# Performance work log

Measured on AMD Instinct MI355X. Metric: run time of the kernel, lower is better.

Reference implementation:

```python
import jax, jax.numpy as jnp
import numpy as np

N_NODES = 50000
DIM = 128
NEG_SLOPE = 0.2


def _gat_conv(x, W, a_src, a_dst, b, src, dst, n):
    # PyG GATConv, single head, self-loops already appended to (src, dst).
    h = x @ W.T                              # [N, D]
    asrc = h @ a_src                         # [N]
    adst = h @ a_dst                         # [N]
    e = jax.nn.leaky_relu(asrc[src] + adst[dst], NEG_SLOPE)  # [E]
    emax = jax.ops.segment_max(e, dst, num_segments=n)
    emax = jnp.where(jnp.isfinite(emax), emax, 0.0)
    ex = jnp.exp(e - emax[dst])
    denom = jax.ops.segment_sum(ex, dst, num_segments=n)
    coef = ex / (denom[dst] + 1e-16)         # segment softmax over incoming edges
    out = jax.ops.segment_sum(coef[:, None] * h[src], dst, num_segments=n)
    return out + b


def _l2norm(x):
    # F.normalize(x) row-wise, eps=1e-12
    n = jnp.sqrt(jnp.sum(x * x, axis=1, keepdims=True))
    return x / jnp.maximum(n, 1e-12)


def setup_inputs() -> dict:
    key = jax.random.key(0)
    ks = jax.random.split(key, 24)
    d = DIM
    inp = {
        'entity_feat_1': jax.random.normal(ks[0], (N_NODES, d), jnp.float32),
        'image_feat': jax.random.normal(ks[1], (N_NODES, 4096), jnp.float32),
        'text_feat': jax.random.normal(ks[2], (N_NODES, 768), jnp.float32),
        'graph_edges': jax.random.randint(ks[3], (2, 600000), 0, N_NODES, jnp.int64),
        'entity_feat': jax.random.normal(ks[4], (N_NODES, d), jnp.float32) * (6.0 / (N_NODES + d)) ** 0.5 * 100,
        'W_img': jax.random.normal(ks[5], (d, 4096), jnp.float32) * 0.02,
        'b_img': jnp.zeros((d,), jnp.float32),
        'W_txt': jax.random.normal(ks[6], (d, 768), jnp.float32) * 0.03,
        'b_txt': jnp.zeros((d,), jnp.float32),
        'W_fus': jax.random.normal(ks[7], (d, 3 * d), jnp.float32) * 0.05,
        'b_fus': jnp.zeros((d,), jnp.float32),
    }
    for i, tag in enumerate(['e', 'i', 't']):
        base = 8 + 4 * i
        inp['W%s_gat' % tag] = jax.random.normal(ks[base], (d, d), jnp.float32) * 0.08
        inp['a%s_src' % tag] = jax.random.normal(ks[base + 1], (d,), jnp.float32) * 0.1
        inp['a%s_dst' % tag] = jax.random.normal(ks[base + 2], (d,), jnp.float32) * 0.1
        inp['b%s_gat' % tag] = jnp.zeros((d,), jnp.float32)
    return inp


def reference(entity_feat_1, image_feat, text_feat, graph_edges, entity_feat,
              W_img, b_img, W_txt, b_txt, W_fus, b_fus,
              We_gat, ae_src, ae_dst, be_gat,
              Wi_gat, ai_src, ai_dst, bi_gat,
              Wt_gat, at_src, at_dst, bt_gat):
    n = entity_feat.shape[0]
    loops = jnp.arange(n, dtype=graph_edges.dtype)
    src = jnp.concatenate([graph_edges[0], loops])
    dst = jnp.concatenate([graph_edges[1], loops])
    img = image_feat @ W_img.T + b_img
    txt = text_feat @ W_txt.T + b_txt
    # GraphConv = GATConv -> dropout(eval: identity) -> F.normalize
    e_out = _l2norm(_gat_conv(entity_feat, We_gat, ae_src, ae_dst, be_gat, src, dst, n))
    i_out = _l2norm(_gat_conv(img, Wi_gat, ai_src, ai_dst, bi_gat, src, dst, n))
    t_out = _l2norm(_gat_conv(txt, Wt_gat, at_src, at_dst, bt_gat, src, dst, n))
    mm = jnp.concatenate([e_out, i_out, t_out], axis=1) @ W_fus.T + b_fus
    return (e_out, i_out, t_out, mm)
```

## Files before the change

kernel.cpp:

```cpp
#include <hip/hip_runtime.h>
#include <hip/hip_bf16.h>

typedef __attribute__((ext_vector_type(8))) short bf16x8;
typedef __attribute__((ext_vector_type(4))) short bf16x4;
typedef __attribute__((ext_vector_type(4))) float f32x4;

#define LDS_A2 16384
#define LDS_HALF2 32768

__device__ __forceinline__ float fin(float v) {
    return (v == v && v > -1e30f && v < 1e30f) ? v : 0.f;
}
__device__ __forceinline__ float lrelu(float v) {
    return (v >= 0.f) ? v : 0.2f * v;
}
__device__ __forceinline__ unsigned f2bu(float f) {
    unsigned u = __builtin_bit_cast(unsigned, f);
    return (u + 0x7FFFu + ((u >> 16) & 1u)) >> 16;
}
__device__ __forceinline__ short f2b(float f) { return (short)f2bu(f); }
__device__ __forceinline__ float bflo(unsigned u) {
    return __builtin_bit_cast(float, u << 16);
}
__device__ __forceinline__ float bfhi(unsigned u) {
    return __builtin_bit_cast(float, u & 0xffff0000u);
}

template<int FUSE, int AD, int HP, int NT, int AF16, int OUT16>
__device__ __forceinline__
void gemm_body(const float* __restrict__ A0, const float* __restrict__ A1,
               const float* __restrict__ A2, const __hip_bfloat16* __restrict__ A16,
               const __hip_bfloat16* __restrict__ Bw,
               const float* __restrict__ bias,
               const float* __restrict__ av1, const float* __restrict__ av2,
               float* __restrict__ asrc, float* __restrict__ adst, int astride,
               float* __restrict__ Cf, __hip_bfloat16* __restrict__ C16,
               unsigned* __restrict__ Cp,
               int M, int K, int bx)
{
    __shared__ __align__(16) char smem[2][LDS_HALF2];
    const int tid = threadIdx.x;
    const int l  = tid & 63;
    const int lr = l & 15;
    const int lk = l >> 4;
    const int w  = tid >> 6;
    const int brow = bx * 128;
    const int nt = K >> 6;

    f32x4 acc[8];
#pragma unroll
    for (int j = 0; j < 8; j++) acc[j] = (f32x4){0.f, 0.f, 0.f, 0.f};

    f32x4 va[4];
    bf16x8 va16[2], vb16[2];

    auto stage_load = [&](int t) {
        const int k0 = t << 6;
        if (AF16) {
#pragma unroll
            for (int i = 0; i < 2; i++) {
                int elem = (i * 512 + tid) * 8;
                int row = elem >> 6;
                int col = elem & 63;
                int gr = brow + row; if (gr >= M) gr = M - 1;
                va16[i] = *(const bf16x8*)(A16 + (size_t)gr * (size_t)K + k0 + col);
            }
        } else {
#pragma unroll
            for (int i = 0; i < 4; i++) {
                int elem = (i * 512 + tid) * 4;
                int row = elem >> 6;
                int col = elem & 63;
                int gr = brow + row; if (gr >= M) gr = M - 1;
                int gcol = k0 + col;
                const float* p;
                if (FUSE) {
                    int seg = gcol >> 7;
                    const float* s = (seg == 0) ? A0 : (seg == 1) ? A1 : A2;
                    p = s + (size_t)gr * 128 + (gcol & 127);
                } else {
                    p = A0 + (size_t)gr * (size_t)K + gcol;
                }
                va[i] = NT ? __builtin_nontemporal_load((const f32x4*)p)
                           : *(const f32x4*)p;
            }
        }
#pragma unroll
        for (int i = 0; i < 2; i++) {
            int elem = (i * 512 + tid) * 8;
            int row = elem >> 6;
            int col = elem & 63;
            vb16[i] = *(const bf16x8*)(Bw + (size_t)row * (size_t)K + k0 + col);
        }
    };
    auto stage_write = [&](int buf) {
        if (AF16) {
#pragma unroll
            for (int i = 0; i < 2; i++) {
                int elem = (i * 512 + tid) * 8;
                int row = elem >> 6;
                int col = elem & 63;
                int slo = (col * 2) ^ ((row & 7) << 4);
                *(bf16x8*)(&smem[buf][row * 128 + slo]) = va16[i];
            }
        } else {
#pragma unroll
            for (int i = 0; i < 4; i++) {
                int elem = (i * 512 + tid) * 4;
                int row = elem >> 6;
                int col = elem & 63;
                int slo = (col * 2) ^ ((row & 7) << 4);
                bf16x4 a4 = {f2b(va[i].x), f2b(va[i].y), f2b(va[i].z), f2b(va[i].w)};
                *(bf16x4*)(&smem[buf][row * 128 + slo]) = a4;
            }
        }
#pragma unroll
        for (int i = 0; i < 2; i++) {
            int elem = (i * 512 + tid) * 8;
            int row = elem >> 6;
            int col = elem & 63;
            int slo = (col * 2) ^ ((row & 7) << 4);
            *(bf16x8*)(&smem[buf][LDS_A2 + row * 128 + slo]) = vb16[i];
        }
    };

    stage_load(0);
    stage_write(0);
    __syncthreads();
    int cur = 0;
    for (int t = 0; t < nt; t++) {
        if (t + 1 < nt) stage_load(t + 1);
        const char* Ab = &smem[cur][0];
        const char* Bb = &smem[cur][LDS_A2];
#pragma unroll
        for (int ks = 0; ks < 2; ks++) {
            bf16x8 af, bv[8];
            {
                int row = w * 16 + lr;
                int lo  = (ks * 64 + lk * 16) ^ ((row & 7) << 4);
                af = *(const bf16x8*)(Ab + row * 128 + lo);
            }
#pragma unroll
            for (int nf = 0; nf < 8; nf++) {
                int row = nf * 16 + lr;
                int lo  = (ks * 64 + lk * 16) ^ ((row & 7) << 4);
                bv[nf] = *(const bf16x8*)(Bb + row * 128 + lo);
            }
#pragma unroll
            for (int nf = 0; nf < 8; nf++)
                acc[nf] = __builtin_amdgcn_mfma_f32_16x16x32_bf16(
                    af, bv[nf], acc[nf], 0, 0, 0);
        }
        if (t + 1 < nt) stage_write(cur ^ 1);
        __syncthreads();
        cur ^= 1;
    }

#pragma unroll
    for (int j = 0; j < 4; j++) {
        int row = brow + w * 16 + lk * 4 + j;
        float vv[8];
        float s1 = 0.f, s2 = 0.f;
#pragma unroll
        for (int nf = 0; nf < 8; nf++) {
            int col = nf * 16 + lr;
            float v = acc[nf][j];
            if (bias) v += bias[col];
            v = fin(v);
            vv[nf] = v;
            if (AD) { s1 += v * av1[col]; s2 += v * av2[col]; }
            if (!HP && !OUT16 && row < M) Cf[(size_t)row * 128 + col] = v;
            if (OUT16 && row < M)
                C16[(size_t)row * 128 + col] = __builtin_bit_cast(__hip_bfloat16, f2b(v));
        }
        if (HP && row < M) {
#pragma unroll
            for (int nf = 0; nf < 4; nf++) {
                int col = nf * 16 + lr;
                Cp[(size_t)row * 64 + col] = f2bu(vv[nf]) | (f2bu(vv[nf + 4]) << 16);
            }
        }
        if (AD) {
#pragma unroll
            for (int o = 1; o < 16; o <<= 1) {
                s1 += __shfl_xor(s1, o);
                s2 += __shfl_xor(s2, o);
            }
            if (lr == 0 && row < M) {
                asrc[(size_t)row * astride] = fin(s1);
                adst[(size_t)row * astride] = fin(s2);
            }
        }
    }
}

__global__ __launch_bounds__(512, 4)
void gemm_o16(const float* __restrict__ A0, const __hip_bfloat16* __restrict__ Bw,
              const float* __restrict__ bias, __hip_bfloat16* __restrict__ C16,
              int M, int K)
{
    gemm_body<0, 0, 0, 1, 0, 1>(A0, nullptr, nullptr, nullptr, Bw, bias,
                                nullptr, nullptr, nullptr, nullptr, 1,
                                nullptr, C16, nullptr, M, K, blockIdx.x);
}

__global__ __launch_bounds__(512, 4)
void gemm_fus(const float* __restrict__ A0, const float* __restrict__ A1,
              const float* __restrict__ A2, const __hip_bfloat16* __restrict__ Bw,
              const float* __restrict__ bias, float* __restrict__ Cf, int M)
{
    gemm_body<1, 0, 0, 0, 0, 0>(A0, A1, A2, nullptr, Bw, bias,
                                nullptr, nullptr, nullptr, nullptr, 1,
                                Cf, nullptr, nullptr, M, 384, blockIdx.x);
}

__global__ __launch_bounds__(512, 4)
void hgemm3(const float* __restrict__ x0, const __hip_bfloat16* __restrict__ x1,
            const __hip_bfloat16* __restrict__ x2,
            const __hip_bfloat16* __restrict__ w0, const __hip_bfloat16* __restrict__ w1,
            const __hip_bfloat16* __restrict__ w2,
            const float* __restrict__ a10, const float* __restrict__ a11,
            const float* __restrict__ a12,
            const float* __restrict__ a20, const float* __restrict__ a21,
            const float* __restrict__ a22,
            unsigned* __restrict__ cp0, unsigned* __restrict__ cp1,
            unsigned* __restrict__ cp2,
            float* __restrict__ asrc4, float* __restrict__ adst4, int M)
{
    int g = blockIdx.y;
    if (g == 0)
        gemm_body<0, 1, 1, 1, 0, 0>(x0, nullptr, nullptr, nullptr, w0, nullptr,
                                    a10, a20, asrc4 + 0, adst4 + 0, 4,
                                    nullptr, nullptr, cp0, M, 128, blockIdx.x);
    else if (g == 1)
        gemm_body<0, 1, 1, 0, 1, 0>(nullptr, nullptr, nullptr, x1, w1, nullptr,
                                    a11, a21, asrc4 + 1, adst4 + 1, 4,
                                    nullptr, nullptr, cp1, M, 128, blockIdx.x);
    else
        gemm_body<0, 1, 1, 0, 1, 0>(nullptr, nullptr, nullptr, x2, w2, nullptr,
                                    a12, a22, asrc4 + 2, adst4 + 2, 4,
                                    nullptr, nullptr, cp2, M, 128, blockIdx.x);
}

__global__ void k_cvt6(const float* __restrict__ s0, const float* __restrict__ s1,
                       const float* __restrict__ s2, const float* __restrict__ s3,
                       const float* __restrict__ s4, const float* __restrict__ s5,
                       __hip_bfloat16* __restrict__ d0, __hip_bfloat16* __restrict__ d1,
                       __hip_bfloat16* __restrict__ d2, __hip_bfloat16* __restrict__ d3,
                       __hip_bfloat16* __restrict__ d4, __hip_bfloat16* __restrict__ d5,
                       int n0, int n1, int n2, int n3, int n4, int n5)
{
    int g = blockIdx.y;
    const float* s = (g == 0) ? s0 : (g == 1) ? s1 : (g == 2) ? s2
                   : (g == 3) ? s3 : (g == 4) ? s4 : s5;
    __hip_bfloat16* d = (g == 0) ? d0 : (g == 1) ? d1 : (g == 2) ? d2
                      : (g == 3) ? d3 : (g == 4) ? d4 : d5;
    int n = (g == 0) ? n0 : (g == 1) ? n1 : (g == 2) ? n2
          : (g == 3) ? n3 : (g == 4) ? n4 : n5;
    for (int i = blockIdx.x * blockDim.x + threadIdx.x; i * 4 < n;
         i += gridDim.x * blockDim.x) {
        f32x4 v = *(const f32x4*)(s + (size_t)i * 4);
        bf16x4 b = {f2b(v.x), f2b(v.y), f2b(v.z), f2b(v.w)};
        *(bf16x4*)((short*)d + (size_t)i * 4) = b;
    }
}

__global__ void k_init(const int* __restrict__ e, int* __restrict__ flag,
                       int* __restrict__ deg, int* __restrict__ cursor, int n)
{
    if (blockIdx.x == 0 && threadIdx.x < 64) {
        int v = e[2 * threadIdx.x + 1];
        unsigned long long b = __ballot(v != 0);
        if (threadIdx.x == 0) flag[0] = (b == 0ull) ? 1 : 0;
    }
    for (int i = blockIdx.x * blockDim.x + threadIdx.x; i < n;
         i += gridDim.x * blockDim.x) {
        deg[i] = 0;
        cursor[i] = 0;
    }
}

__global__ void k_degree(const int* __restrict__ e, const int* __restrict__ flag,
                         int* __restrict__ deg, int e0, int n)
{
    int i = blockIdx.x * blockDim.x + threadIdx.x;
    if (i >= e0 + n) return;
    int d;
    if (i < e0) d = flag[0] ? e[2 * e0 + 2 * i] : e[e0 + i];
    else        d = i - e0;
    if ((unsigned)d >= (unsigned)n) d = 0;
    atomicAdd(&deg[d], 1);
}

__global__ void k_scan1(const int* __restrict__ deg, int* __restrict__ csum, int n)
{
    __shared__ int sh[512];
    int c = blockIdx.x, t = threadIdx.x, i = c * 512 + t;
    sh[t] = (i < n) ? deg[i] : 0;
    __syncthreads();
    for (int o = 256; o; o >>= 1) {
        if (t < o) sh[t] += sh[t + o];
        __syncthreads();
    }
    if (t == 0) csum[c] = sh[0];
}

__global__ void k_scan2(const int* __restrict__ csum, int* __restrict__ coff,
                        int nc, int* __restrict__ indptr, int n, int total)
{
    __shared__ int sh[128];
    int t = threadIdx.x;
    int v = (t < nc) ? csum[t] : 0;
    sh[t] = v;
    __syncthreads();
    for (int o = 1; o < 128; o <<= 1) {
        int add = (t >= o) ? sh[t - o] : 0;
        __syncthreads();
        sh[t] += add;
        __syncthreads();
    }
    if (t < nc) coff[t] = sh[t] - v;
    if (t == 0) indptr[n] = total;
}

__global__ void k_scan3(const int* __restrict__ deg, const int* __restrict__ coff,
                        int* __restrict__ indptr, int n)
{
    __shared__ int sh[512];
    int c = blockIdx.x, t = threadIdx.x, i = c * 512 + t;
    int v = (i < n) ? deg[i] : 0;
    sh[t] = v;
    __syncthreads();
    for (int o = 1; o < 512; o <<= 1) {
        int add = (t >= o) ? sh[t - o] : 0;
        __syncthreads();
        sh[t] += add;
        __syncthreads();
    }
    if (i < n) indptr[i] = coff[c] + sh[t] - v;
}

__global__ void k_scatter(const int* __restrict__ e, const int* __restrict__ flag,
                          const int* __restrict__ indptr,
                          int* __restrict__ cursor, int* __restrict__ csr,
                          int e0, int n)
{
    int i = blockIdx.x * blockDim.x + threadIdx.x;
    if (i >= e0 + n) return;
    int s, d;
    if (i < e0) {
        if (flag[0]) { s = e[2 * i]; d = e[2 * e0 + 2 * i]; }
        else         { s = e[i];     d = e[e0 + i]; }
    } else {
        s = d = i - e0;
    }
    if ((unsigned)d >= (unsigned)n) d = 0;
    if ((unsigned)s >= (unsigned)n) s = 0;
    int pos = atomicAdd(&cursor[d], 1);
    csr[indptr[d] + pos] = s;
}

__global__ __launch_bounds__(256)
void gat3(const int* __restrict__ indptr, const int* __restrict__ csr,
          const unsigned* __restrict__ hpE, const unsigned* __restrict__ hpI,
          const unsigned* __restrict__ hpT,
          const float* __restrict__ asrc4, const float* __restrict__ adst4,
          const float* __restrict__ bE, const float* __restrict__ bI,
          const float* __restrict__ bT,
          float* __restrict__ oE, float* __restrict__ oI, float* __restrict__ oT,
          int n)
{
    int node = blockIdx.x * 4 + (threadIdx.x >> 6);
    if (node >= n) return;
    int l = threadIdx.x & 63;
    int beg = indptr[node], end = indptr[node + 1];
    int deg_n = end - beg;
    float adE = adst4[(size_t)node * 4 + 0];
    float adI = adst4[(size_t)node * 4 + 1];
    float adT = adst4[(size_t)node * 4 + 2];
    float aE0 = 0.f, aE1 = 0.f, aI0 = 0.f, aI1 = 0.f, aT0 = 0.f, aT1 = 0.f;

    if (deg_n <= 64) {
        int t = beg + l;
        bool valid = t < end;
        int sidx = valid ? csr[t] : 0;
        if ((unsigned)sidx >= (unsigned)n) sidx = 0;
        float eE = -1e30f, eI = -1e30f, eT = -1e30f;
        if (valid) {
            const float* ap = asrc4 + (size_t)sidx * 4;
            eE = lrelu(ap[0] + adE);
            eI = lrelu(ap[1] + adI);
            eT = lrelu(ap[2] + adT);
        }
        float mE = eE, mI = eI, mT = eT;
        for (int o = 32; o; o >>= 1) {
            mE = fmaxf(mE, __shfl_xor(mE, o));
            mI = fmaxf(mI, __shfl_xor(mI, o));
            mT = fmaxf(mT, __shfl_xor(mT, o));
        }
        float xE = valid ? __expf(eE - mE) : 0.f;
        float xI = valid ? __expf(eI - mI) : 0.f;
        float xT = valid ? __expf(eT - mT) : 0.f;
        float sE = xE, sI = xI, sT = xT;
        for (int o = 32; o; o >>= 1) {
            sE += __shfl_xor(sE, o);
            sI += __shfl_xor(sI, o);
            sT += __shfl_xor(sT, o);
        }
        float iE = 1.f / (sE + 1e-16f);
        float iI = 1.f / (sI + 1e-16f);
        float iT = 1.f / (sT + 1e-16f);
        for (int j = 0; j < deg_n; j++) {
            int   sj = __shfl(sidx, j);
            float cE = __shfl(xE, j) * iE;
            float cI = __shfl(xI, j) * iI;
            float cT = __shfl(xT, j) * iT;
            unsigned uE = hpE[(size_t)sj * 64 + l];
            unsigned uI = hpI[(size_t)sj * 64 + l];
            unsigned uT = hpT[(size_t)sj * 64 + l];
            aE0 += cE * bflo(uE); aE1 += cE * bfhi(uE);
            aI0 += cI * bflo(uI); aI1 += cI * bfhi(uI);
            aT0 += cT * bflo(uT); aT1 += cT * bfhi(uT);
        }
    } else {
        const unsigned* hp[3] = {hpE, hpI, hpT};
        float ad3[3] = {adE, adI, adT};
        float* acc0[3] = {&aE0, &aI0, &aT0};
        float* acc1[3] = {&aE1, &aI1, &aT1};
        for (int g = 0; g < 3; g++) {
            float m = -1e30f;
            for (int t = beg + l; t < end; t += 64) {
                int sidx = csr[t];
                if ((unsigned)sidx >= (unsigned)n) sidx = 0;
                m = fmaxf(m, lrelu(asrc4[(size_t)sidx * 4 + g] + ad3[g]));
            }
            for (int o = 32; o; o >>= 1) m = fmaxf(m, __shfl_xor(m, o));
            float s = 0.f;
            for (int t = beg + l; t < end; t += 64) {
                int sidx = csr[t];
                if ((unsigned)sidx >= (unsigned)n) sidx = 0;
                s += __expf(lrelu(asrc4[(size_t)sidx * 4 + g] + ad3[g]) - m);
            }
            for (int o = 32; o; o >>= 1) s += __shfl_xor(s, o);
            float inv = 1.f / (s + 1e-16f);
            for (int t = beg; t < end; t++) {
                int sidx = csr[t];
                if ((unsigned)sidx >= (unsigned)n) sidx = 0;
                float c = __expf(lrelu(asrc4[(size_t)sidx * 4 + g] + ad3[g]) - m) * inv;
                unsigned u = hp[g][(size_t)sidx * 64 + l];
                *acc0[g] += c * bflo(u);
                *acc1[g] += c * bfhi(u);
            }
        }
    }

    {
        float a0 = aE0 + bE[l], a1 = aE1 + bE[64 + l];
        float ss = a0 * a0 + a1 * a1;
        for (int o = 32; o; o >>= 1) ss += __shfl_xor(ss, o);
        float r = 1.f / fmaxf(sqrtf(fin(ss)), 1e-12f);
        oE[(size_t)node * 128 + l]      = fin(a0 * r);
        oE[(size_t)node * 128 + 64 + l] = fin(a1 * r);
    }
    {
        float a0 = aI0 + bI[l], a1 = aI1 + bI[64 + l];
        float ss = a0 * a0 + a1 * a1;
        for (int o = 32; o; o >>= 1) ss += __shfl_xor(ss, o);
        float r = 1.f / fmaxf(sqrtf(fin(ss)), 1e-12f);
        oI[(size_t)node * 128 + l]      = fin(a0 * r);
        oI[(size_t)node * 128 + 64 + l] = fin(a1 * r);
    }
    {
        float a0 = aT0 + bT[l], a1 = aT1 + bT[64 + l];
        float ss = a0 * a0 + a1 * a1;
        for (int o = 32; o; o >>= 1) ss += __shfl_xor(ss, o);
        float r = 1.f / fmaxf(sqrtf(fin(ss)), 1e-12f);
        oT[(size_t)node * 128 + l]      = fin(a0 * r);
        oT[(size_t)node * 128 + 64 + l] = fin(a1 * r);
    }
}

extern "C" void kernel_launch(void* const* d_in, const int* in_sizes, int n_in,
                              void* d_out, int out_size, void* d_ws, size_t ws_size,
                              hipStream_t stream)
{
    int s0 = n_in - 22;
    if (s0 < 0 || s0 > 1)
        s0 = (in_sizes[1] > in_sizes[0]) ? 1 : 0;

    const float* image_feat  = (const float*)d_in[s0 + 0];
    const float* text_feat   = (const float*)d_in[s0 + 1];
    const int*   edges       = (const int*)d_in[s0 + 2];
    const float* entity_feat = (const float*)d_in[s0 + 3];
    const float* W_img = (const float*)d_in[s0 + 4];
    const float* b_img = (const float*)d_in[s0 + 5];
    const float* W_txt = (const float*)d_in[s0 + 6];
    const float* b_txt = (const float*)d_in[s0 + 7];
    const float* W_fus = (const float*)d_in[s0 + 8];
    const float* b_fus = (const float*)d_in[s0 + 9];
    const float* Wg[3]  = {(const float*)d_in[s0 + 10], (const float*)d_in[s0 + 14],
                           (const float*)d_in[s0 + 18]};
    const float* Avv[3] = {(const float*)d_in[s0 + 11], (const float*)d_in[s0 + 15],
                           (const float*)d_in[s0 + 19]};
    const float* Dvv[3] = {(const float*)d_in[s0 + 12], (const float*)d_in[s0 + 16],
                           (const float*)d_in[s0 + 20]};
    const float* Bg[3]  = {(const float*)d_in[s0 + 13], (const float*)d_in[s0 + 17],
                           (const float*)d_in[s0 + 21]};

    const int n  = in_sizes[s0 + 3] / 128;
    int e0 = in_sizes[s0 + 2] / 2;
    if (e0 == 24 * n) e0 = 12 * n;
    const int ne = e0 + n;
    const int Kimg = in_sizes[s0 + 4] / 128;
    const int Ktxt = in_sizes[s0 + 6] / 128;

    char* ws = (char*)d_ws;
    size_t off = 0;
    auto alloc = [&](size_t b) { size_t o = off; off = (off + b + 255) & ~(size_t)255; return o; };
    int* eflag  = (int*)(ws + alloc(256));
    int* deg    = (int*)(ws + alloc((size_t)n * 4));
    int* indptr = (int*)(ws + alloc((size_t)(n + 1) * 4));
    int* cursor = (int*)(ws + alloc((size_t)n * 4));
    int* csum   = (int*)(ws + alloc(512));
    int* coff   = (int*)(ws + alloc(512));
    float* asrc4 = (float*)(ws + alloc((size_t)n * 16));
    float* adst4 = (float*)(ws + alloc((size_t)n * 16));
    int* csr    = (int*)(ws + alloc((size_t)ne * 4));
    __hip_bfloat16* Wimgb = (__hip_bfloat16*)(ws + alloc((size_t)Kimg * 128 * 2));
    __hip_bfloat16* Wtxtb = (__hip_bfloat16*)(ws + alloc((size_t)Ktxt * 128 * 2));
    __hip_bfloat16* Wgb[3];
    for (int g = 0; g < 3; g++) Wgb[g] = (__hip_bfloat16*)(ws + alloc(128 * 128 * 2));
    __hip_bfloat16* Wfusb = (__hip_bfloat16*)(ws + alloc(384 * 128 * 2));
    __hip_bfloat16* imgp16 = (__hip_bfloat16*)(ws + alloc((size_t)n * 128 * 2));
    __hip_bfloat16* txtp16 = (__hip_bfloat16*)(ws + alloc((size_t)n * 128 * 2));
    unsigned* hp[3];
    for (int g = 0; g < 3; g++) hp[g] = (unsigned*)(ws + alloc((size_t)n * 64 * 4));
    (void)ws_size; (void)out_size;

    float* out = (float*)d_out;
    float* oE = out;
    float* oI = out + (size_t)n * 128;
    float* oT = out + 2 * (size_t)n * 128;
    float* oM = out + 3 * (size_t)n * 128;

    k_init<<<208, 256, 0, stream>>>(edges, eflag, deg, cursor, n);
    k_cvt6<<<dim3(128, 6), 256, 0, stream>>>(
        W_img, W_txt, Wg[0], Wg[1], Wg[2], W_fus,
        Wimgb, Wtxtb, Wgb[0], Wgb[1], Wgb[2], Wfusb,
        Kimg * 128, Ktxt * 128, 128 * 128, 128 * 128, 128 * 128, 384 * 128);
    k_degree<<<(ne + 255) / 256, 256, 0, stream>>>(edges, eflag, deg, e0, n);
    const int nch = (n + 511) / 512;
    k_scan1<<<nch, 512, 0, stream>>>(deg, csum, n);
    k_scan2<<<1, 128, 0, stream>>>(csum, coff, nch, indptr, n, ne);
    k_scan3<<<nch, 512, 0, stream>>>(deg, coff, indptr, n);
    k_scatter<<<(ne + 255) / 256, 256, 0, stream>>>(edges, eflag, indptr, cursor, csr, e0, n);

    const int mb = (n + 127) / 128;
    gemm_o16<<<mb, 512, 0, stream>>>(image_feat, Wimgb, b_img, imgp16, n, Kimg);
    gemm_o16<<<mb, 512, 0, stream>>>(text_feat, Wtxtb, b_txt, txtp16, n, Ktxt);

    hgemm3<<<dim3(mb, 3), 512, 0, stream>>>(entity_feat, imgp16, txtp16,
                                            Wgb[0], Wgb[1], Wgb[2],
                                            Avv[0], Avv[1], Avv[2],
                                            Dvv[0], Dvv[1], Dvv[2],
                                            hp[0], hp[1], hp[2],
                                            asrc4, adst4, n);

    gat3<<<(n + 3) / 4, 256, 0, stream>>>(indptr, csr, hp[0], hp[1], hp[2],
                                          asrc4, adst4, Bg[0], Bg[1], Bg[2],
                                          oE, oI, oT, n);

    gemm_fus<<<mb, 512, 0, stream>>>(oE, oI, oT, Wfusb, b_fus, oM, n);
}
```

Baseline: 437.7 us.

## Compose projection and GAT weights to fuse the two GEMM stages into one

Precomputes Wg·W_img and Wg·W_txt (and the composed biases) on device, so the GAT linear transform for the image and text branches runs straight from the raw features in a single GEMM launch. This removes the intermediate bf16 projection buffers and the second GEMM pass over them. The three per-branch h buffers are also interleaved into one 192-word-per-node layout so the GAT gather reads one contiguous region per source node. The trade-offs are an added weight-composition kernel and different rounding, since the intermediate projection is no longer rounded to bf16. The large image and text GEMMs now share one launch grid with the small entity GEMM.

```diff
diff --git a/kernel.cpp b/kernel.cpp
--- a/kernel.cpp
+++ b/kernel.cpp
@@ -26,16 +26,15 @@
     return __builtin_bit_cast(float, u & 0xffff0000u);
 }
 
-template<int FUSE, int AD, int HP, int NT, int AF16, int OUT16>
+template<int FUSE, int AD, int HP, int NT>
 __device__ __forceinline__
 void gemm_body(const float* __restrict__ A0, const float* __restrict__ A1,
-               const float* __restrict__ A2, const __hip_bfloat16* __restrict__ A16,
+               const float* __restrict__ A2,
                const __hip_bfloat16* __restrict__ Bw,
                const float* __restrict__ bias,
                const float* __restrict__ av1, const float* __restrict__ av2,
                float* __restrict__ asrc, float* __restrict__ adst, int astride,
-               float* __restrict__ Cf, __hip_bfloat16* __restrict__ C16,
-               unsigned* __restrict__ Cp,
+               float* __restrict__ Cf, unsigned* __restrict__ Cp, int cpstride,
                int M, int K, int bx)
 {
     __shared__ __align__(16) char smem[2][LDS_HALF2];
@@ -52,38 +51,27 @@
     for (int j = 0; j < 8; j++) acc[j] = (f32x4){0.f, 0.f, 0.f, 0.f};
 
     f32x4 va[4];
-    bf16x8 va16[2], vb16[2];
+    bf16x8 vb16[2];
 
     auto stage_load = [&](int t) {
         const int k0 = t << 6;
-        if (AF16) {
-#pragma unroll
-            for (int i = 0; i < 2; i++) {
-                int elem = (i * 512 + tid) * 8;
-                int row = elem >> 6;
-                int col = elem & 63;
-                int gr = brow + row; if (gr >= M) gr = M - 1;
-                va16[i] = *(const bf16x8*)(A16 + (size_t)gr * (size_t)K + k0 + col);
-            }
-        } else {
-#pragma unroll
-            for (int i = 0; i < 4; i++) {
-                int elem = (i * 512 + tid) * 4;
-                int row = elem >> 6;
-                int col = elem & 63;
-                int gr = brow + row; if (gr >= M) gr = M - 1;
-                int gcol = k0 + col;
-                const float* p;
-                if (FUSE) {
-                    int seg = gcol >> 7;
-                    const float* s = (seg == 0) ? A0 : (seg == 1) ? A1 : A2;
-                    p = s + (size_t)gr * 128 + (gcol & 127);
-                } else {
-                    p = A0 + (size_t)gr * (size_t)K + gcol;
-                }
-                va[i] = NT ? __builtin_nontemporal_load((const f32x4*)p)
-                           : *(const f32x4*)p;
-            }
+#pragma unroll
+        for (int i = 0; i < 4; i++) {
+            int elem = (i * 512 + tid) * 4;
+            int row = elem >> 6;
+            int col = elem & 63;
+            int gr = brow + row; if (gr >= M) gr = M - 1;
+            int gcol = k0 + col;
+            const float* p;
+            if (FUSE) {
+                int seg = gcol >> 7;
+                const float* s = (seg == 0) ? A0 : (seg == 1) ? A1 : A2;
+                p = s + (size_t)gr * 128 + (gcol & 127);
+            } else {
+                p = A0 + (size_t)gr * (size_t)K + gcol;
+            }
+            va[i] = NT ? __builtin_nontemporal_load((const f32x4*)p)
+                       : *(const f32x4*)p;
         }
 #pragma unroll
         for (int i = 0; i < 2; i++) {
@@ -94,25 +82,14 @@
         }
     };
     auto stage_write = [&](int buf) {
-        if (AF16) {
-#pragma unroll
-            for (int i = 0; i < 2; i++) {
-                int elem = (i * 512 + tid) * 8;
-                int row = elem >> 6;
-                int col = elem & 63;
-                int slo = (col * 2) ^ ((row & 7) << 4);
-                *(bf16x8*)(&smem[buf][row * 128 + slo]) = va16[i];
-            }
-        } else {
-#pragma unroll
-            for (int i = 0; i < 4; i++) {
-                int elem = (i * 512 + tid) * 4;
-                int row = elem >> 6;
-                int col = elem & 63;
-                int slo = (col * 2) ^ ((row & 7) << 4);
-                bf16x4 a4 = {f2b(va[i].x), f2b(va[i].y), f2b(va[i].z), f2b(va[i].w)};
-                *(bf16x4*)(&smem[buf][row * 128 + slo]) = a4;
-            }
+#pragma unroll
+        for (int i = 0; i < 4; i++) {
+            int elem = (i * 512 + tid) * 4;
+            int row = elem >> 6;
+            int col = elem & 63;
+            int slo = (col * 2) ^ ((row & 7) << 4);
+            bf16x4 a4 = {f2b(va[i].x), f2b(va[i].y), f2b(va[i].z), f2b(va[i].w)};
+            *(bf16x4*)(&smem[buf][row * 128 + slo]) = a4;
         }
 #pragma unroll
         for (int i = 0; i < 2; i++) {
@@ -169,15 +146,13 @@
             v = fin(v);
             vv[nf] = v;
             if (AD) { s1 += v * av1[col]; s2 += v * av2[col]; }
-            if (!HP && !OUT16 && row < M) Cf[(size_t)row * 128 + col] = v;
-            if (OUT16 && row < M)
-                C16[(size_t)row * 128 + col] = __builtin_bit_cast(__hip_bfloat16, f2b(v));
+            if (!HP && row < M) Cf[(size_t)row * 128 + col] = v;
         }
         if (HP && row < M) {
 #pragma unroll
             for (int nf = 0; nf < 4; nf++) {
                 int col = nf * 16 + lr;
-                Cp[(size_t)row * 64 + col] = f2bu(vv[nf]) | (f2bu(vv[nf + 4]) << 16);
+                Cp[(size_t)row * cpstride + col] = f2bu(vv[nf]) | (f2bu(vv[nf + 4]) << 16);
             }
         }
         if (AD) {
@@ -195,13 +170,30 @@
 }
 
 __global__ __launch_bounds__(512, 4)
-void gemm_o16(const float* __restrict__ A0, const __hip_bfloat16* __restrict__ Bw,
-              const float* __restrict__ bias, __hip_bfloat16* __restrict__ C16,
-              int M, int K)
-{
-    gemm_body<0, 0, 0, 1, 0, 1>(A0, nullptr, nullptr, nullptr, Bw, bias,
-                                nullptr, nullptr, nullptr, nullptr, 1,
-                                nullptr, C16, nullptr, M, K, blockIdx.x);
+void hgemm3b(const float* __restrict__ x0, const float* __restrict__ x1,
+             const float* __restrict__ x2,
+             const __hip_bfloat16* __restrict__ w0,
+             const __hip_bfloat16* __restrict__ w1,
+             const __hip_bfloat16* __restrict__ w2,
+             const float* __restrict__ bc1, const float* __restrict__ bc2,
+             const float* __restrict__ a10, const float* __restrict__ a11,
+             const float* __restrict__ a12,
+             const float* __restrict__ a20, const float* __restrict__ a21,
+             const float* __restrict__ a22,
+             unsigned* __restrict__ hpAll,
+             float* __restrict__ asrc4, float* __restrict__ adst4,
+             int M, int K0, int K1, int K2)
+{
+    int g = blockIdx.y;
+    const float* x  = (g == 0) ? x0 : (g == 1) ? x1 : x2;
+    const __hip_bfloat16* wv = (g == 0) ? w0 : (g == 1) ? w1 : w2;
+    const float* bias = (g == 0) ? nullptr : (g == 1) ? bc1 : bc2;
+    const float* av1 = (g == 0) ? a10 : (g == 1) ? a11 : a12;
+    const float* av2 = (g == 0) ? a20 : (g == 1) ? a21 : a22;
+    int K = (g == 0) ? K0 : (g == 1) ? K1 : K2;
+    gemm_body<0, 1, 1, 1>(x, nullptr, nullptr, wv, bias, av1, av2,
+                          asrc4 + g, adst4 + g, 4,
+                          nullptr, hpAll + g * 64, 192, M, K, blockIdx.x);
 }
 
 __global__ __launch_bounds__(512, 4)
@@ -209,54 +201,66 @@
               const float* __restrict__ A2, const __hip_bfloat16* __restrict__ Bw,
               const float* __restrict__ bias, float* __restrict__ Cf, int M)
 {
-    gemm_body<1, 0, 0, 0, 0, 0>(A0, A1, A2, nullptr, Bw, bias,
-                                nullptr, nullptr, nullptr, nullptr, 1,
-                                Cf, nullptr, nullptr, M, 384, blockIdx.x);
-}
-
-__global__ __launch_bounds__(512, 4)
-void hgemm3(const float* __restrict__ x0, const __hip_bfloat16* __restrict__ x1,
-            const __hip_bfloat16* __restrict__ x2,
-            const __hip_bfloat16* __restrict__ w0, const __hip_bfloat16* __restrict__ w1,
-            const __hip_bfloat16* __restrict__ w2,
-            const float* __restrict__ a10, const float* __restrict__ a11,
-            const float* __restrict__ a12,
-            const float* __restrict__ a20, const float* __restrict__ a21,
-            const float* __restrict__ a22,
-            unsigned* __restrict__ cp0, unsigned* __restrict__ cp1,
-            unsigned* __restrict__ cp2,
-            float* __restrict__ asrc4, float* __restrict__ adst4, int M)
+    gemm_body<1, 0, 0, 0>(A0, A1, A2, Bw, bias, nullptr, nullptr,
+                          nullptr, nullptr, 1, Cf, nullptr, 1, M, 384, blockIdx.x);
+}
+
+__global__ __launch_bounds__(256)
+void k_compose(const float* __restrict__ Wg1, const float* __restrict__ Wb1,
+               const float* __restrict__ bb1, __hip_bfloat16* __restrict__ Wc1,
+               float* __restrict__ bc1, int K1,
+               const float* __restrict__ Wg2, const float* __restrict__ Wb2,
+               const float* __restrict__ bb2, __hip_bfloat16* __restrict__ Wc2,
+               float* __restrict__ bc2, int K2)
+{
+    int y = blockIdx.y;
+    const float* Wg  = y ? Wg2 : Wg1;
+    const float* Wb  = y ? Wb2 : Wb1;
+    const float* bb  = y ? bb2 : bb1;
+    __hip_bfloat16* Wc = y ? Wc2 : Wc1;
+    float* bc = y ? bc2 : bc1;
+    int Kbig = y ? K2 : K1;
+    int tid = threadIdx.x;
+
+    if (blockIdx.x == gridDim.x - 1) {
+        __shared__ float bs[128];
+        if (tid < 128) bs[tid] = bb[tid];
+        __syncthreads();
+        if (tid < 128) {
+            float s = 0.f;
+            for (int m = 0; m < 128; m++) s = fmaf(Wg[tid * 128 + m], bs[m], s);
+            bc[tid] = fin(s);
+        }
+        return;
+    }
+    __shared__ float WgL[128 * 128];
+    for (int i = tid; i < 128 * 128; i += 256) WgL[i] = Wg[i];
+    __syncthreads();
+    int j = blockIdx.x * 64 + (tid & 63);
+    if (j >= Kbig) return;
+    int g = tid >> 6;
+    float acc[32];
+#pragma unroll
+    for (int i = 0; i < 32; i++) acc[i] = 0.f;
+    for (int k = 0; k < 128; k++) {
+        float wvv = Wb[(size_t)k * Kbig + j];
+#pragma unroll
+        for (int i = 0; i < 32; i++)
+            acc[i] = fmaf(WgL[(g * 32 + i) * 128 + k], wvv, acc[i]);
+    }
+#pragma unroll
+    for (int i = 0; i < 32; i++)
+        *((short*)Wc + (size_t)(g * 32 + i) * Kbig + j) = f2b(acc[i]);
+}
+
+__global__ void k_cvt2(const float* __restrict__ s0, const float* __restrict__ s1,
+                       __hip_bfloat16* __restrict__ d0, __hip_bfloat16* __restrict__ d1,
+                       int n0, int n1)
 {
     int g = blockIdx.y;
-    if (g == 0)
-        gemm_body<0, 1, 1, 1, 0, 0>(x0, nullptr, nullptr, nullptr, w0, nullptr,
-                                    a10, a20, asrc4 + 0, adst4 + 0, 4,
-                                    nullptr, nullptr, cp0, M, 128, blockIdx.x);
-    else if (g == 1)
-        gemm_body<0, 1, 1, 0, 1, 0>(nullptr, nullptr, nullptr, x1, w1, nullptr,
-                                    a11, a21, asrc4 + 1, adst4 + 1, 4,
-                                    nullptr, nullptr, cp1, M, 128, blockIdx.x);
-    else
-        gemm_body<0, 1, 1, 0, 1, 0>(nullptr, nullptr, nullptr, x2, w2, nullptr,
-                                    a12, a22, asrc4 + 2, adst4 + 2, 4,
-                                    nullptr, nullptr, cp2, M, 128, blockIdx.x);
-}
-
-__global__ void k_cvt6(const float* __restrict__ s0, const float* __restrict__ s1,
-                       const float* __restrict__ s2, const float* __restrict__ s3,
-                       const float* __restrict__ s4, const float* __restrict__ s5,
-                       __hip_bfloat16* __restrict__ d0, __hip_bfloat16* __restrict__ d1,
-                       __hip_bfloat16* __restrict__ d2, __hip_bfloat16* __restrict__ d3,
-                       __hip_bfloat16* __restrict__ d4, __hip_bfloat16* __restrict__ d5,
-                       int n0, int n1, int n2, int n3, int n4, int n5)
-{
-    int g = blockIdx.y;
-    const float* s = (g == 0) ? s0 : (g == 1) ? s1 : (g == 2) ? s2
-                   : (g == 3) ? s3 : (g == 4) ? s4 : s5;
-    __hip_bfloat16* d = (g == 0) ? d0 : (g == 1) ? d1 : (g == 2) ? d2
-                      : (g == 3) ? d3 : (g == 4) ? d4 : d5;
-    int n = (g == 0) ? n0 : (g == 1) ? n1 : (g == 2) ? n2
-          : (g == 3) ? n3 : (g == 4) ? n4 : n5;
+    const float* s = g ? s1 : s0;
+    __hip_bfloat16* d = g ? d1 : d0;
+    int n = g ? n1 : n0;
     for (int i = blockIdx.x * blockDim.x + threadIdx.x; i * 4 < n;
          i += gridDim.x * blockDim.x) {
         f32x4 v = *(const f32x4*)(s + (size_t)i * 4);
@@ -362,8 +366,7 @@
 
 __global__ __launch_bounds__(256)
 void gat3(const int* __restrict__ indptr, const int* __restrict__ csr,
-          const unsigned* __restrict__ hpE, const unsigned* __restrict__ hpI,
-          const unsigned* __restrict__ hpT,
+          const unsigned* __restrict__ hpAll,
           const float* __restrict__ asrc4, const float* __restrict__ adst4,
           const float* __restrict__ bE, const float* __restrict__ bI,
           const float* __restrict__ bT,
@@ -415,15 +418,15 @@
             float cE = __shfl(xE, j) * iE;
             float cI = __shfl(xI, j) * iI;
             float cT = __shfl(xT, j) * iT;
-            unsigned uE = hpE[(size_t)sj * 64 + l];
-            unsigned uI = hpI[(size_t)sj * 64 + l];
-            unsigned uT = hpT[(size_t)sj * 64 + l];
+            const unsigned* hb = hpAll + (size_t)sj * 192;
+            unsigned uE = hb[l];
+            unsigned uI = hb[64 + l];
+            unsigned uT = hb[128 + l];
             aE0 += cE * bflo(uE); aE1 += cE * bfhi(uE);
             aI0 += cI * bflo(uI); aI1 += cI * bfhi(uI);
             aT0 += cT * bflo(uT); aT1 += cT * bfhi(uT);
         }
     } else {
-        const unsigned* hp[3] = {hpE, hpI, hpT};
         float ad3[3] = {adE, adI, adT};
         float* acc0[3] = {&aE0, &aI0, &aT0};
         float* acc1[3] = {&aE1, &aI1, &aT1};
@@ -447,7 +450,7 @@
                 int sidx = csr[t];
                 if ((unsigned)sidx >= (unsigned)n) sidx = 0;
                 float c = __expf(lrelu(asrc4[(size_t)sidx * 4 + g] + ad3[g]) - m) * inv;
-                unsigned u = hp[g][(size_t)sidx * 64 + l];
+                unsigned u = hpAll[(size_t)sidx * 192 + g * 64 + l];
                 *acc0[g] += c * bflo(u);
                 *acc1[g] += c * bfhi(u);
             }
@@ -526,15 +529,13 @@
     float* asrc4 = (float*)(ws + alloc((size_t)n * 16));
     float* adst4 = (float*)(ws + alloc((size_t)n * 16));
     int* csr    = (int*)(ws + alloc((size_t)ne * 4));
-    __hip_bfloat16* Wimgb = (__hip_bfloat16*)(ws + alloc((size_t)Kimg * 128 * 2));
-    __hip_bfloat16* Wtxtb = (__hip_bfloat16*)(ws + alloc((size_t)Ktxt * 128 * 2));
-    __hip_bfloat16* Wgb[3];
-    for (int g = 0; g < 3; g++) Wgb[g] = (__hip_bfloat16*)(ws + alloc(128 * 128 * 2));
+    __hip_bfloat16* Wgb0  = (__hip_bfloat16*)(ws + alloc(128 * 128 * 2));
     __hip_bfloat16* Wfusb = (__hip_bfloat16*)(ws + alloc(384 * 128 * 2));
-    __hip_bfloat16* imgp16 = (__hip_bfloat16*)(ws + alloc((size_t)n * 128 * 2));
-    __hip_bfloat16* txtp16 = (__hip_bfloat16*)(ws + alloc((size_t)n * 128 * 2));
-    unsigned* hp[3];
-    for (int g = 0; g < 3; g++) hp[g] = (unsigned*)(ws + alloc((size_t)n * 64 * 4));
+    __hip_bfloat16* Wcimg = (__hip_bfloat16*)(ws + alloc((size_t)Kimg * 128 * 2));
+    __hip_bfloat16* Wctxt = (__hip_bfloat16*)(ws + alloc((size_t)Ktxt * 128 * 2));
+    float* bcimg = (float*)(ws + alloc(512));
+    float* bctxt = (float*)(ws + alloc(512));
+    unsigned* hpAll = (unsigned*)(ws + alloc((size_t)n * 192 * 4));
     (void)ws_size; (void)out_size;
 
     float* out = (float*)d_out;
@@ -544,10 +545,11 @@
     float* oM = out + 3 * (size_t)n * 128;
 
     k_init<<<208, 256, 0, stream>>>(edges, eflag, deg, cursor, n);
-    k_cvt6<<<dim3(128, 6), 256, 0, stream>>>(
-        W_img, W_txt, Wg[0], Wg[1], Wg[2], W_fus,
-        Wimgb, Wtxtb, Wgb[0], Wgb[1], Wgb[2], Wfusb,
-        Kimg * 128, Ktxt * 128, 128 * 128, 128 * 128, 128 * 128, 384 * 128);
+    k_cvt2<<<dim3(64, 2), 256, 0, stream>>>(Wg[0], W_fus, Wgb0, Wfusb,
+                                            128 * 128, 384 * 128);
+    k_compose<<<dim3(Kimg / 64 + 1, 2), 256, 0, stream>>>(
+        Wg[1], W_img, b_img, Wcimg, bcimg, Kimg,
+        Wg[2], W_txt, b_txt, Wctxt, bctxt, Ktxt);
     k_degree<<<(ne + 255) / 256, 256, 0, stream>>>(edges, eflag, deg, e0, n);
     const int nch = (n + 511) / 512;
     k_scan1<<<nch, 512, 0, stream>>>(deg, csum, n);
@@ -556,17 +558,14 @@
     k_scatter<<<(ne + 255) / 256, 256, 0, stream>>>(edges, eflag, indptr, cursor, csr, e0, n);
 
     const int mb = (n + 127) / 128;
-    gemm_o16<<<mb, 512, 0, stream>>>(image_feat, Wimgb, b_img, imgp16, n, Kimg);
-    gemm_o16<<<mb, 512, 0, stream>>>(text_feat, Wtxtb, b_txt, txtp16, n, Ktxt);
-
-    hgemm3<<<dim3(mb, 3), 512, 0, stream>>>(entity_feat, imgp16, txtp16,
-                                            Wgb[0], Wgb[1], Wgb[2],
-                                            Avv[0], Avv[1], Avv[2],
-                                            Dvv[0], Dvv[1], Dvv[2],
-                                            hp[0], hp[1], hp[2],
-                                            asrc4, adst4, n);
-
-    gat3<<<(n + 3) / 4, 256, 0, stream>>>(indptr, csr, hp[0], hp[1], hp[2],
+    hgemm3b<<<dim3(mb, 3), 512, 0, stream>>>(entity_feat, image_feat, text_feat,
+                                             Wgb0, Wcimg, Wctxt, bcimg, bctxt,
+                                             Avv[0], Avv[1], Avv[2],
+                                             Dvv[0], Dvv[1], Dvv[2],
+                                             hpAll, asrc4, adst4,
+                                             n, 128, Kimg, Ktxt);
+
+    gat3<<<(n + 3) / 4, 256, 0, stream>>>(indptr, csr, hpAll,
                                           asrc4, adst4, Bg[0], Bg[1], Bg[2],
                                           oE, oI, oT, n);
 
```

Result: slower. 452.6 us (+3.4%).
